# Performance work log

Measured on AMD Instinct MI355X. Metric: run time of the kernel, lower is better.

## Reference

```python
import jax, jax.numpy as jnp
import numpy as np

D = 3072      # hidden_dim == flattened CIFAR image size
KF = 1        # FourierFeature k (default, KAN_FourierAttention does not pass k)
NP = 5        # module-level n -> size of w and n parameter vectors
NC = 100      # num_classes
B = 512


def setup_inputs() -> dict:
    key = jax.random.key(0)
    ks = jax.random.split(key, 7)
    return {
        "x": jax.random.normal(ks[0], (B, 3, 32, 32), dtype=jnp.float32),
        "a": jax.random.normal(ks[1], (D, D, KF), dtype=jnp.float32),
        "b": jax.random.normal(ks[2], (D, D, KF), dtype=jnp.float32),
        "w": jax.random.normal(ks[3], (NP,), dtype=jnp.float32),
        "n_param": jax.random.normal(ks[4], (NP,), dtype=jnp.float32),
        "fc_w": jax.random.normal(ks[5], (NC, D), dtype=jnp.float32) * 0.02,
        "fc_b": jax.random.normal(ks[6], (NC,), dtype=jnp.float32) * 0.02,
    }


def reference(x, a, b, w, n_param, fc_w, fc_b):
    xf = x.reshape(x.shape[0], -1)                 # [B, D]
    m = jnp.arange(1, KF + 1, dtype=xf.dtype)      # [KF]
    cos_part = jnp.cos(xf[..., None] * m)          # [B, D, KF]
    sin_part = jnp.sin(xf[..., None] * m)          # [B, D, KF]
    # Original: result[b,i,j] = sum_k cos[b,j,k]*a[i,j,k] + sin[b,j,k]*b[i,j,k]
    # then part2[b,j] = sum_i result[b,i,j].  Fuse both reductions (over i and k)
    # to avoid materializing the [B, D, D, KF] broadcast intermediate.
    part2 = (jnp.einsum('bdk,idk->bd', cos_part, a)
             + jnp.einsum('bdk,idk->bd', sin_part, b))   # [B, D]
    # part1: scalar accumulated over i=1..len(n)-1
    part1 = jnp.sum(w[1:] * n_param[1:] + w[:-1] * n_param[:-1])
    Z = part1 + part2                               # [B, D]
    return Z @ fc_w.T + fc_b                        # [B, NC]
```

## Files before the change

### kernel.cpp

```cpp
#include <hip/hip_runtime.h>
#include <math.h>

#define D 3072
#define BATCH 512
#define NCLS 100
#define KS 32
#define KCHUNK (D / KS)
#define RC 96

typedef __attribute__((ext_vector_type(8))) short bf16x8;
typedef __attribute__((ext_vector_type(4))) float f32x4;

#define WS_OFF_W   2359296
#define WS_OFF_P   3047424
#define WS_NEED    (WS_OFF_P + (size_t)KS * BATCH * NCLS * 2)

__device__ inline unsigned short f2bf(float f) {
    unsigned u = __float_as_uint(f);
    u += 0x7FFF + ((u >> 16) & 1);
    return (unsigned short)(u >> 16);
}
__device__ inline float bf2f(unsigned short s) {
    return __uint_as_float(((unsigned)s) << 16);
}

__global__ __launch_bounds__(256) void prep_kernel(const float* __restrict__ a,
                                                   const float* __restrict__ b,
                                                   const float* __restrict__ fcw,
                                                   float* __restrict__ pws,
                                                   unsigned short* __restrict__ Wb) {
    const int bid = blockIdx.x;
    const int t   = threadIdx.x;
    if (bid < 288) {
        const int rc   = bid / 3;
        const int cg   = bid % 3;
        const int col  = cg * 1024 + t * 4;
        const int row0 = rc * 32;
        float4 sa = make_float4(0.f, 0.f, 0.f, 0.f);
        float4 sb = make_float4(0.f, 0.f, 0.f, 0.f);
        #pragma unroll
        for (int r = 0; r < 32; ++r) {
            const int i = row0 + r;
            const float4 va = *(const float4*)(a + i * D + col);
            const float4 vb = *(const float4*)(b + i * D + col);
            sa.x += va.x; sa.y += va.y; sa.z += va.z; sa.w += va.w;
            sb.x += vb.x; sb.y += vb.y; sb.z += vb.z; sb.w += vb.w;
        }
        *(float4*)(pws + rc * D + col)            = sa;
        *(float4*)(pws + (RC + rc) * D + col)     = sb;
    } else {
        const int idx = (bid - 288) * 256 + t;
        const int c   = idx / (D / 4);
        const int d   = (idx % (D / 4)) * 4;
        ushort4 o;
        if (c < NCLS) {
            const float4 v = *(const float4*)(fcw + c * D + d);
            o.x = f2bf(v.x); o.y = f2bf(v.y); o.z = f2bf(v.z); o.w = f2bf(v.w);
        } else {
            o.x = o.y = o.z = o.w = 0;
        }
        *(ushort4*)(Wb + c * D + d) = o;
    }
}

__global__ __launch_bounds__(256) void fzgemm_kernel(
        const float* __restrict__ x,
        const float* __restrict__ w5,
        const float* __restrict__ n5,
        const float* __restrict__ pws,
        const unsigned short* __restrict__ Wb,
        unsigned short* __restrict__ part) {
    __shared__ float Al[KCHUNK];
    __shared__ float Bl[KCHUNK];

    const int t    = threadIdx.x;
    const int wave = t >> 6;
    const int lane = t & 63;
    const int l16  = lane & 15;
    const int quad = lane >> 4;
    const int m0   = blockIdx.x * 64 + wave * 16;
    const int j    = blockIdx.y;
    const int cbase = j * KCHUNK;

    if (t < KCHUNK) {
        float s = 0.f;
        #pragma unroll 8
        for (int rc = 0; rc < RC; ++rc)
            s += pws[rc * D + cbase + t];
        Al[t] = s;
    } else if (t >= 128 && t < 128 + KCHUNK) {
        const int c = t - 128;
        float s = 0.f;
        #pragma unroll 8
        for (int rc = 0; rc < RC; ++rc)
            s += pws[(RC + rc) * D + cbase + c];
        Bl[c] = s;
    }

    float part1 = 0.f;
    #pragma unroll
    for (int i = 0; i < 4; ++i)
        part1 += w5[i + 1] * n5[i + 1] + w5[i] * n5[i];

    f32x4 acc[7];
    #pragma unroll
    for (int n = 0; n < 7; ++n) acc[n] = (f32x4){0.f, 0.f, 0.f, 0.f};

    const float* xr = x + (m0 + l16) * D;
    __syncthreads();

    #pragma unroll
    for (int kk = 0; kk < KCHUNK; kk += 32) {
        const int lcol = quad * 8 + kk;
        const int gcol = cbase + lcol;
        const float4 xv0 = *(const float4*)(xr + gcol);
        const float4 xv1 = *(const float4*)(xr + gcol + 4);
        const float4 Av0 = *(const float4*)&Al[lcol];
        const float4 Av1 = *(const float4*)&Al[lcol + 4];
        const float4 Bv0 = *(const float4*)&Bl[lcol];
        const float4 Bv1 = *(const float4*)&Bl[lcol + 4];

        union { bf16x8 v; unsigned short s[8]; } af;
        float sv, cv;
        __sincosf(xv0.x, &sv, &cv); af.s[0] = f2bf(part1 + cv * Av0.x + sv * Bv0.x);
        __sincosf(xv0.y, &sv, &cv); af.s[1] = f2bf(part1 + cv * Av0.y + sv * Bv0.y);
        __sincosf(xv0.z, &sv, &cv); af.s[2] = f2bf(part1 + cv * Av0.z + sv * Bv0.z);
        __sincosf(xv0.w, &sv, &cv); af.s[3] = f2bf(part1 + cv * Av0.w + sv * Bv0.w);
        __sincosf(xv1.x, &sv, &cv); af.s[4] = f2bf(part1 + cv * Av1.x + sv * Bv1.x);
        __sincosf(xv1.y, &sv, &cv); af.s[5] = f2bf(part1 + cv * Av1.y + sv * Bv1.y);
        __sincosf(xv1.z, &sv, &cv); af.s[6] = f2bf(part1 + cv * Av1.z + sv * Bv1.z);
        __sincosf(xv1.w, &sv, &cv); af.s[7] = f2bf(part1 + cv * Av1.w + sv * Bv1.w);

        #pragma unroll
        for (int n = 0; n < 7; ++n) {
            const bf16x8 bf = *(const bf16x8*)(Wb + (n * 16 + l16) * D + gcol);
            acc[n] = __builtin_amdgcn_mfma_f32_16x16x32_bf16(af.v, bf, acc[n], 0, 0, 0);
        }
    }

    unsigned short* pb = part + (size_t)j * (BATCH * NCLS);
    #pragma unroll
    for (int n = 0; n < 7; ++n) {
        const int c = n * 16 + l16;
        if (c < NCLS) {
            #pragma unroll
            for (int r = 0; r < 4; ++r)
                pb[(m0 + quad * 4 + r) * NCLS + c] = f2bf(acc[n][r]);
        }
    }
}

__global__ __launch_bounds__(256) void reduce2_kernel(
        const unsigned int* __restrict__ partu,
        const float* __restrict__ fcb,
        float* __restrict__ out) {
    const int idx = blockIdx.x * 256 + threadIdx.x;
    const int c   = (idx * 2) % NCLS;
    float s0 = fcb[c];
    float s1 = fcb[c + 1];
    #pragma unroll
    for (int ks = 0; ks < KS; ++ks) {
        const unsigned int v = partu[ks * (BATCH * NCLS / 2) + idx];
        s0 += bf2f((unsigned short)(v & 0xFFFF));
        s1 += bf2f((unsigned short)(v >> 16));
    }
    *(float2*)(out + idx * 2) = make_float2(s0, s1);
}

__global__ __launch_bounds__(256) void colsum_atomic_kernel(
        const float* __restrict__ a, const float* __restrict__ b,
        float* __restrict__ ws) {
    const int col  = (blockIdx.x % 3) * 1024 + threadIdx.x * 4;
    const int row0 = (blockIdx.x / 3) * 32;
    float4 sa = make_float4(0.f, 0.f, 0.f, 0.f);
    float4 sb = make_float4(0.f, 0.f, 0.f, 0.f);
    #pragma unroll
    for (int r = 0; r < 32; ++r) {
        const float4 va = *(const float4*)(a + (row0 + r) * D + col);
        const float4 vb = *(const float4*)(b + (row0 + r) * D + col);
        sa.x += va.x; sa.y += va.y; sa.z += va.z; sa.w += va.w;
        sb.x += vb.x; sb.y += vb.y; sb.z += vb.z; sb.w += vb.w;
    }
    atomicAdd(&ws[col + 0], sa.x); atomicAdd(&ws[col + 1], sa.y);
    atomicAdd(&ws[col + 2], sa.z); atomicAdd(&ws[col + 3], sa.w);
    atomicAdd(&ws[D + col + 0], sb.x); atomicAdd(&ws[D + col + 1], sb.y);
    atomicAdd(&ws[D + col + 2], sb.z); atomicAdd(&ws[D + col + 3], sb.w);
}

__global__ __launch_bounds__(256) void fused_gemm_kernel(
        const float* __restrict__ x,
        const float* __restrict__ w5,
        const float* __restrict__ n5,
        const float* __restrict__ fcw,
        const float* __restrict__ fcb,
        const float* __restrict__ ws,
        float* __restrict__ out) {
    __shared__ __align__(16) float Zl[32 * 36];
    __shared__ __align__(16) float Wl[32 * 132];
    const int t  = threadIdx.x;
    const int bt = blockIdx.x;
    const int j  = blockIdx.y;
    float part1 = 0.f;
    #pragma unroll
    for (int i = 0; i < 4; ++i)
        part1 += w5[i + 1] * n5[i + 1] + w5[i] * n5[i];
    const int c0 = (t & 31) * 4;
    const int b0 = (t >> 5) * 4;
    const int kl = t & 31;
    const int tg = t >> 5;
    const int bbase = bt * 32;
    float acc[4][4];
    #pragma unroll
    for (int i = 0; i < 4; ++i)
        #pragma unroll
        for (int q = 0; q < 4; ++q) acc[i][q] = 0.f;
    for (int s = 0; s < 3; ++s) {
        const int dbase = j * 96 + s * 32;
        for (int idx = t; idx < NCLS * 32; idx += 256) {
            const int c = idx >> 5;
            const int k = idx & 31;
            Wl[k * 132 + c] = fcw[c * D + dbase + k];
        }
        const float Av = ws[dbase + kl];
        const float Bv = ws[D + dbase + kl];
        #pragma unroll
        for (int i = 0; i < 4; ++i) {
            const int bl = tg + i * 8;
            const float xv = x[(bbase + bl) * D + dbase + kl];
            float sv, cv;
            sincosf(xv, &sv, &cv);
            Zl[bl * 36 + kl] = part1 + cv * Av + sv * Bv;
        }
        __syncthreads();
        #pragma unroll
        for (int k = 0; k < 32; ++k) {
            const float4 wv = *(const float4*)&Wl[k * 132 + c0];
            float zb[4];
            #pragma unroll
            for (int bj = 0; bj < 4; ++bj) zb[bj] = Zl[(b0 + bj) * 36 + k];
            #pragma unroll
            for (int bj = 0; bj < 4; ++bj) {
                acc[bj][0] += zb[bj] * wv.x;
                acc[bj][1] += zb[bj] * wv.y;
                acc[bj][2] += zb[bj] * wv.z;
                acc[bj][3] += zb[bj] * wv.w;
            }
        }
        __syncthreads();
    }
    if (c0 < NCLS) {
        #pragma unroll
        for (int bj = 0; bj < 4; ++bj) {
            const int row = bbase + b0 + bj;
            #pragma unroll
            for (int q = 0; q < 4; ++q) {
                const int c = c0 + q;
                if (c < NCLS) {
                    float v = acc[bj][q];
                    if (j == 0) v += fcb[c];
                    atomicAdd(&out[row * NCLS + c], v);
                }
            }
        }
    }
}

extern "C" void kernel_launch(void* const* d_in, const int* in_sizes, int n_in,
                              void* d_out, int out_size, void* d_ws, size_t ws_size,
                              hipStream_t stream) {
    const float* x   = (const float*)d_in[0];
    const float* a   = (const float*)d_in[1];
    const float* b   = (const float*)d_in[2];
    const float* w5  = (const float*)d_in[3];
    const float* n5  = (const float*)d_in[4];
    const float* fcw = (const float*)d_in[5];
    const float* fcb = (const float*)d_in[6];
    float* out = (float*)d_out;
    float* wsf = (float*)d_ws;

    if (ws_size >= WS_NEED) {
        unsigned short* Wb = (unsigned short*)((char*)d_ws + WS_OFF_W);
        unsigned short* Pp = (unsigned short*)((char*)d_ws + WS_OFF_P);
        prep_kernel<<<dim3(624), 256, 0, stream>>>(a, b, fcw, wsf, Wb);
        fzgemm_kernel<<<dim3(8, KS), 256, 0, stream>>>(x, w5, n5, wsf, Wb, Pp);
        reduce2_kernel<<<dim3(100), 256, 0, stream>>>((const unsigned int*)Pp,
                                                      fcb, out);
    } else {
        hipMemsetAsync(d_ws, 0, 2 * D * sizeof(float), stream);
        hipMemsetAsync(d_out, 0, (size_t)out_size * sizeof(float), stream);
        colsum_atomic_kernel<<<dim3(288), 256, 0, stream>>>(a, b, wsf);
        fused_gemm_kernel<<<dim3(16, 32), 256, 0, stream>>>(x, w5, n5, fcw, fcb,
                                                            wsf, out);
    }
}
```

Baseline: 127.9 us.

## Split column-sum into more blocks, add separate reduce stage, widen GEMM split-K

Column-sum partials now use 768 blocks of 12 rows instead of 288 blocks of 32 rows, and a new csred kernel folds them into final column sums once. This replaces the per-block redundant reduction that each fzgemm block did before. The GEMM split-K grows from 32 to 96 chunks, so each block does a single 32-wide MFMA step. Partials are stored in fp32, which makes the intermediate buffer larger, and the final reduce uses 4 threads per output pair. The cost is one extra kernel launch and more partial-sum traffic in the final reduction.

```diff
diff --git a/kernel.cpp b/kernel.cpp
--- a/kernel.cpp
+++ b/kernel.cpp
@@ -4,16 +4,16 @@
 #define D 3072
 #define BATCH 512
 #define NCLS 100
-#define KS 32
-#define KCHUNK (D / KS)
-#define RC 96
+#define RC12 256
+#define KS 96
 
 typedef __attribute__((ext_vector_type(8))) short bf16x8;
 typedef __attribute__((ext_vector_type(4))) float f32x4;
 
-#define WS_OFF_W   2359296
-#define WS_OFF_P   3047424
-#define WS_NEED    (WS_OFF_P + (size_t)KS * BATCH * NCLS * 2)
+#define WS_OFF_CS  6291456ULL
+#define WS_OFF_W   6316032ULL
+#define WS_OFF_P   7004160ULL
+#define WS_NEED    (WS_OFF_P + (size_t)KS * BATCH * NCLS * 4)
 
 __device__ inline unsigned short f2bf(float f) {
     unsigned u = __float_as_uint(f);
@@ -31,48 +31,66 @@
                                                    unsigned short* __restrict__ Wb) {
     const int bid = blockIdx.x;
     const int t   = threadIdx.x;
-    if (bid < 288) {
+    if (bid < 768) {
         const int rc   = bid / 3;
         const int cg   = bid % 3;
         const int col  = cg * 1024 + t * 4;
-        const int row0 = rc * 32;
+        const int row0 = rc * 12;
         float4 sa = make_float4(0.f, 0.f, 0.f, 0.f);
         float4 sb = make_float4(0.f, 0.f, 0.f, 0.f);
         #pragma unroll
-        for (int r = 0; r < 32; ++r) {
+        for (int r = 0; r < 12; ++r) {
             const int i = row0 + r;
-            const float4 va = *(const float4*)(a + i * D + col);
-            const float4 vb = *(const float4*)(b + i * D + col);
+            const float4 va = *(const float4*)(a + (size_t)i * D + col);
+            const float4 vb = *(const float4*)(b + (size_t)i * D + col);
             sa.x += va.x; sa.y += va.y; sa.z += va.z; sa.w += va.w;
             sb.x += vb.x; sb.y += vb.y; sb.z += vb.z; sb.w += vb.w;
         }
-        *(float4*)(pws + rc * D + col)            = sa;
-        *(float4*)(pws + (RC + rc) * D + col)     = sb;
+        *(float4*)(pws + (size_t)rc * D + col)          = sa;
+        *(float4*)(pws + (size_t)(RC12 + rc) * D + col) = sb;
     } else {
-        const int idx = (bid - 288) * 256 + t;
-        const int c   = idx / (D / 4);
-        const int d   = (idx % (D / 4)) * 4;
-        ushort4 o;
-        if (c < NCLS) {
-            const float4 v = *(const float4*)(fcw + c * D + d);
-            o.x = f2bf(v.x); o.y = f2bf(v.y); o.z = f2bf(v.z); o.w = f2bf(v.w);
-        } else {
-            o.x = o.y = o.z = o.w = 0;
-        }
-        *(ushort4*)(Wb + c * D + d) = o;
-    }
+        const int base = ((bid - 768) * 256 + t) * 2;
+        #pragma unroll
+        for (int u = 0; u < 2; ++u) {
+            const int idx = base + u;
+            const int c   = idx / (D / 4);
+            const int d   = (idx % (D / 4)) * 4;
+            ushort4 o;
+            if (c < NCLS) {
+                const float4 v = *(const float4*)(fcw + (size_t)c * D + d);
+                o.x = f2bf(v.x); o.y = f2bf(v.y); o.z = f2bf(v.z); o.w = f2bf(v.w);
+            } else {
+                o.x = o.y = o.z = o.w = 0;
+            }
+            *(ushort4*)(Wb + (size_t)c * D + d) = o;
+        }
+    }
+}
+
+__global__ __launch_bounds__(256) void csred_kernel(const float* __restrict__ pws,
+                                                    float* __restrict__ csF) {
+    const int tid = blockIdx.x * 256 + threadIdx.x;
+    const int i   = tid >> 2;
+    const int g   = tid & 3;
+    const int a2  = i / D;
+    const int col = i % D;
+    const float* p = pws + (size_t)(a2 * RC12 + g * 64) * D + col;
+    float s = 0.f;
+    #pragma unroll 8
+    for (int rc = 0; rc < 64; ++rc)
+        s += p[(size_t)rc * D];
+    s += __shfl_xor(s, 1);
+    s += __shfl_xor(s, 2);
+    if (g == 0) csF[(size_t)a2 * D + col] = s;
 }
 
 __global__ __launch_bounds__(256) void fzgemm_kernel(
         const float* __restrict__ x,
         const float* __restrict__ w5,
         const float* __restrict__ n5,
-        const float* __restrict__ pws,
+        const float* __restrict__ csF,
         const unsigned short* __restrict__ Wb,
-        unsigned short* __restrict__ part) {
-    __shared__ float Al[KCHUNK];
-    __shared__ float Bl[KCHUNK];
-
+        float* __restrict__ part) {
     const int t    = threadIdx.x;
     const int wave = t >> 6;
     const int lane = t & 63;
@@ -80,91 +98,74 @@
     const int quad = lane >> 4;
     const int m0   = blockIdx.x * 64 + wave * 16;
     const int j    = blockIdx.y;
-    const int cbase = j * KCHUNK;
-
-    if (t < KCHUNK) {
-        float s = 0.f;
-        #pragma unroll 8
-        for (int rc = 0; rc < RC; ++rc)
-            s += pws[rc * D + cbase + t];
-        Al[t] = s;
-    } else if (t >= 128 && t < 128 + KCHUNK) {
-        const int c = t - 128;
-        float s = 0.f;
-        #pragma unroll 8
-        for (int rc = 0; rc < RC; ++rc)
-            s += pws[(RC + rc) * D + cbase + c];
-        Bl[c] = s;
-    }
+    const int gcol = j * 32 + quad * 8;
 
     float part1 = 0.f;
     #pragma unroll
     for (int i = 0; i < 4; ++i)
         part1 += w5[i + 1] * n5[i + 1] + w5[i] * n5[i];
 
+    const float4 Av0 = *(const float4*)(csF + gcol);
+    const float4 Av1 = *(const float4*)(csF + gcol + 4);
+    const float4 Bv0 = *(const float4*)(csF + D + gcol);
+    const float4 Bv1 = *(const float4*)(csF + D + gcol + 4);
+
+    const float* xr = x + (size_t)(m0 + l16) * D;
+    const float4 xv0 = *(const float4*)(xr + gcol);
+    const float4 xv1 = *(const float4*)(xr + gcol + 4);
+
+    union { bf16x8 v; unsigned short s[8]; } af;
+    float sv, cv;
+    __sincosf(xv0.x, &sv, &cv); af.s[0] = f2bf(part1 + cv * Av0.x + sv * Bv0.x);
+    __sincosf(xv0.y, &sv, &cv); af.s[1] = f2bf(part1 + cv * Av0.y + sv * Bv0.y);
+    __sincosf(xv0.z, &sv, &cv); af.s[2] = f2bf(part1 + cv * Av0.z + sv * Bv0.z);
+    __sincosf(xv0.w, &sv, &cv); af.s[3] = f2bf(part1 + cv * Av0.w + sv * Bv0.w);
+    __sincosf(xv1.x, &sv, &cv); af.s[4] = f2bf(part1 + cv * Av1.x + sv * Bv1.x);
+    __sincosf(xv1.y, &sv, &cv); af.s[5] = f2bf(part1 + cv * Av1.y + sv * Bv1.y);
+    __sincosf(xv1.z, &sv, &cv); af.s[6] = f2bf(part1 + cv * Av1.z + sv * Bv1.z);
+    __sincosf(xv1.w, &sv, &cv); af.s[7] = f2bf(part1 + cv * Av1.w + sv * Bv1.w);
+
     f32x4 acc[7];
     #pragma unroll
     for (int n = 0; n < 7; ++n) acc[n] = (f32x4){0.f, 0.f, 0.f, 0.f};
-
-    const float* xr = x + (m0 + l16) * D;
-    __syncthreads();
-
-    #pragma unroll
-    for (int kk = 0; kk < KCHUNK; kk += 32) {
-        const int lcol = quad * 8 + kk;
-        const int gcol = cbase + lcol;
-        const float4 xv0 = *(const float4*)(xr + gcol);
-        const float4 xv1 = *(const float4*)(xr + gcol + 4);
-        const float4 Av0 = *(const float4*)&Al[lcol];
-        const float4 Av1 = *(const float4*)&Al[lcol + 4];
-        const float4 Bv0 = *(const float4*)&Bl[lcol];
-        const float4 Bv1 = *(const float4*)&Bl[lcol + 4];
-
-        union { bf16x8 v; unsigned short s[8]; } af;
-        float sv, cv;
-        __sincosf(xv0.x, &sv, &cv); af.s[0] = f2bf(part1 + cv * Av0.x + sv * Bv0.x);
-        __sincosf(xv0.y, &sv, &cv); af.s[1] = f2bf(part1 + cv * Av0.y + sv * Bv0.y);
-        __sincosf(xv0.z, &sv, &cv); af.s[2] = f2bf(part1 + cv * Av0.z + sv * Bv0.z);
-        __sincosf(xv0.w, &sv, &cv); af.s[3] = f2bf(part1 + cv * Av0.w + sv * Bv0.w);
-        __sincosf(xv1.x, &sv, &cv); af.s[4] = f2bf(part1 + cv * Av1.x + sv * Bv1.x);
-        __sincosf(xv1.y, &sv, &cv); af.s[5] = f2bf(part1 + cv * Av1.y + sv * Bv1.y);
-        __sincosf(xv1.z, &sv, &cv); af.s[6] = f2bf(part1 + cv * Av1.z + sv * Bv1.z);
-        __sincosf(xv1.w, &sv, &cv); af.s[7] = f2bf(part1 + cv * Av1.w + sv * Bv1.w);
-
-        #pragma unroll
-        for (int n = 0; n < 7; ++n) {
-            const bf16x8 bf = *(const bf16x8*)(Wb + (n * 16 + l16) * D + gcol);
-            acc[n] = __builtin_amdgcn_mfma_f32_16x16x32_bf16(af.v, bf, acc[n], 0, 0, 0);
-        }
-    }
-
-    unsigned short* pb = part + (size_t)j * (BATCH * NCLS);
+    #pragma unroll
+    for (int n = 0; n < 7; ++n) {
+        const bf16x8 bf = *(const bf16x8*)(Wb + (size_t)(n * 16 + l16) * D + gcol);
+        acc[n] = __builtin_amdgcn_mfma_f32_16x16x32_bf16(af.v, bf, acc[n], 0, 0, 0);
+    }
+
+    float* pb = part + (size_t)j * (BATCH * NCLS);
     #pragma unroll
     for (int n = 0; n < 7; ++n) {
         const int c = n * 16 + l16;
         if (c < NCLS) {
             #pragma unroll
             for (int r = 0; r < 4; ++r)
-                pb[(m0 + quad * 4 + r) * NCLS + c] = f2bf(acc[n][r]);
-        }
-    }
-}
-
-__global__ __launch_bounds__(256) void reduce2_kernel(
-        const unsigned int* __restrict__ partu,
+                pb[(size_t)(m0 + quad * 4 + r) * NCLS + c] = acc[n][r];
+        }
+    }
+}
+
+__global__ __launch_bounds__(256) void reduce_kernel(
+        const float* __restrict__ part,
         const float* __restrict__ fcb,
         float* __restrict__ out) {
-    const int idx = blockIdx.x * 256 + threadIdx.x;
-    const int c   = (idx * 2) % NCLS;
-    float s0 = fcb[c];
-    float s1 = fcb[c + 1];
-    #pragma unroll
-    for (int ks = 0; ks < KS; ++ks) {
-        const unsigned int v = partu[ks * (BATCH * NCLS / 2) + idx];
-        s0 += bf2f((unsigned short)(v & 0xFFFF));
-        s1 += bf2f((unsigned short)(v >> 16));
-    }
-    *(float2*)(out + idx * 2) = make_float2(s0, s1);
+    const int tid = blockIdx.x * 256 + threadIdx.x;
+    const int p   = tid >> 2;
+    const int g   = tid & 3;
+    const int b   = p / (NCLS / 2);
+    const int c   = (p % (NCLS / 2)) * 2;
+    const float* pp = part + (size_t)g * 24 * (BATCH * NCLS) + (size_t)b * NCLS + c;
+    float s0 = 0.f, s1 = 0.f;
+    #pragma unroll 8
+    for (int k = 0; k < 24; ++k) {
+        const float2 v = *(const float2*)(pp + (size_t)k * (BATCH * NCLS));
+        s0 += v.x; s1 += v.y;
+    }
+    s0 += __shfl_xor(s0, 1); s0 += __shfl_xor(s0, 2);
+    s1 += __shfl_xor(s1, 1); s1 += __shfl_xor(s1, 2);
+    if (g == 0)
+        *(float2*)(out + (size_t)b * NCLS + c) = make_float2(s0 + fcb[c], s1 + fcb[c + 1]);
 }
 
 __global__ __launch_bounds__(256) void colsum_atomic_kernel(
@@ -176,8 +177,8 @@
     float4 sb = make_float4(0.f, 0.f, 0.f, 0.f);
     #pragma unroll
     for (int r = 0; r < 32; ++r) {
-        const float4 va = *(const float4*)(a + (row0 + r) * D + col);
-        const float4 vb = *(const float4*)(b + (row0 + r) * D + col);
+        const float4 va = *(const float4*)(a + (size_t)(row0 + r) * D + col);
+        const float4 vb = *(const float4*)(b + (size_t)(row0 + r) * D + col);
         sa.x += va.x; sa.y += va.y; sa.z += va.z; sa.w += va.w;
         sb.x += vb.x; sb.y += vb.y; sb.z += vb.z; sb.w += vb.w;
     }
@@ -219,14 +220,14 @@
         for (int idx = t; idx < NCLS * 32; idx += 256) {
             const int c = idx >> 5;
             const int k = idx & 31;
-            Wl[k * 132 + c] = fcw[c * D + dbase + k];
+            Wl[k * 132 + c] = fcw[(size_t)c * D + dbase + k];
         }
         const float Av = ws[dbase + kl];
         const float Bv = ws[D + dbase + kl];
         #pragma unroll
         for (int i = 0; i < 4; ++i) {
             const int bl = tg + i * 8;
-            const float xv = x[(bbase + bl) * D + dbase + kl];
+            const float xv = x[(size_t)(bbase + bl) * D + dbase + kl];
             float sv, cv;
             sincosf(xv, &sv, &cv);
             Zl[bl * 36 + kl] = part1 + cv * Av + sv * Bv;
@@ -258,7 +259,7 @@
                 if (c < NCLS) {
                     float v = acc[bj][q];
                     if (j == 0) v += fcb[c];
-                    atomicAdd(&out[row * NCLS + c], v);
+                    atomicAdd(&out[(size_t)row * NCLS + c], v);
                 }
             }
         }
@@ -279,12 +280,13 @@
     float* wsf = (float*)d_ws;
 
     if (ws_size >= WS_NEED) {
-        unsigned short* Wb = (unsigned short*)((char*)d_ws + WS_OFF_W);
-        unsigned short* Pp = (unsigned short*)((char*)d_ws + WS_OFF_P);
-        prep_kernel<<<dim3(624), 256, 0, stream>>>(a, b, fcw, wsf, Wb);
-        fzgemm_kernel<<<dim3(8, KS), 256, 0, stream>>>(x, w5, n5, wsf, Wb, Pp);
-        reduce2_kernel<<<dim3(100), 256, 0, stream>>>((const unsigned int*)Pp,
-                                                      fcb, out);
+        float*          csF  = (float*)((char*)d_ws + WS_OFF_CS);
+        unsigned short* Wb   = (unsigned short*)((char*)d_ws + WS_OFF_W);
+        float*          partf = (float*)((char*)d_ws + WS_OFF_P);
+        prep_kernel<<<dim3(936), 256, 0, stream>>>(a, b, fcw, wsf, Wb);
+        csred_kernel<<<dim3(96), 256, 0, stream>>>(wsf, csF);
+        fzgemm_kernel<<<dim3(8, KS), 256, 0, stream>>>(x, w5, n5, csF, Wb, partf);
+        reduce_kernel<<<dim3(400), 256, 0, stream>>>(partf, fcb, out);
     } else {
         hipMemsetAsync(d_ws, 0, 2 * D * sizeof(float), stream);
         hipMemsetAsync(d_out, 0, (size_t)out_size * sizeof(float), stream);
```

Result: no change. 129.6 us (+1.3%).
